# Optimization experiments

Hardware: AMD Instinct MI355X
Metric: run time of the kernel (lower is better)

Reference implementation:

```python
import itertools
import jax, jax.numpy as jnp
import numpy as np

DIM = 3; N_NEIGH = 4096; N_CH = 64
BASIS_RANK_MAX = 2; SELF_TP_RANK_MAX = 2; H_MAX_RANK = 2  # layer=1 -> h_max_rank=2
R_CUT = 5.0  # Bessel radial-basis cutoff (assumed)

def find_combinations(a_max, b_max, s):
    if s > a_max + b_max or s < 0:
        return []
    return [(a, s - a) for a in range(max(0, s - b_max), min(a_max, s) + 1)]

def contraction_is_valid(n_in, n_out):
    # can only reduce legs pairwise (metric contraction)
    return n_in >= n_out and (n_in - n_out) % 2 == 0

def _pairings(legs):
    if not legs:
        yield []
        return
    a = legs[0]
    for i in range(1, len(legs)):
        for rest in _pairings(legs[1:i] + legs[i + 1:]):
            yield [(a, legs[i])] + rest

def contraction_einsums(a, b, c_out):
    # all distinct pairwise contractions of an (a+b)-leg Cartesian tensor down to c_out free legs
    n = a + b
    letters = 'defghijklm'
    eqs = []
    for contracted in itertools.combinations(range(n), n - c_out):
        free = [l for l in range(n) if l not in contracted]
        for match in _pairings(list(contracted)):
            lab = {}
            cnt = 0
            for l in free:
                lab[l] = letters[cnt]; cnt += 1
            for (p, q) in match:
                lab[p] = lab[q] = letters[cnt]; cnt += 1
            s1 = 'nc' + ''.join(lab[l] for l in range(a))
            s2 = 'nc' + ''.join(lab[l] for l in range(a, n))
            so = 'nc' + ''.join(lab[l] for l in free)
            eqs.append(f'{s1},{s2}->{so}')
    return eqs

def tensor_prod(r, order):
    # repeated outer product of unit vectors: (N, dim^order); order 0 -> ones (N,)
    if order == 0:
        return jnp.ones((r.shape[0],), r.dtype)
    out = r
    for _ in range(order - 1):
        out = jnp.einsum('n...,nd->n...d', out, r)
    return out

def e_rbf(r, n):
    # Bessel/sinc radial basis: sqrt(2/c) sin(n pi r / c) / r
    return jnp.sqrt(2.0 / R_CUT) * jnp.sin(n * jnp.pi * r / R_CUT) / r

def setup_inputs() -> dict:
    key = jax.random.key(0)
    ks = jax.random.split(key, 5)
    return {
        'h0': jax.random.normal(ks[0], (N_NEIGH, N_CH), jnp.float32),
        'h1': jax.random.normal(ks[1], (N_NEIGH, N_CH, DIM), jnp.float32),
        'h2': jax.random.normal(ks[2], (N_NEIGH, N_CH, DIM, DIM), jnp.float32),
        'rel_poss': jax.random.normal(ks[3], (N_NEIGH, DIM), jnp.float32),
        'channel_weights': jax.random.normal(ks[4], (BASIS_RANK_MAX + 1, N_NEIGH, N_CH, N_CH), jnp.float32),
    }

def _forward(h0, h1, h2, rel_poss, channel_weights):
    h = [h0, h1, h2]
    dists = jnp.linalg.norm(rel_poss, axis=-1)                  # (N,)
    nrp = rel_poss / dists.reshape(-1, 1)                       # unit vectors (N, 3)
    # channel mixing computed but unused downstream in the original forward (dead code, kept faithful)
    _ = [jnp.einsum('ijk,ik...->ij...', channel_weights[r], h[r]) for r in range(BASIS_RANK_MAX + 1)]
    r_base = [tensor_prod(nrp, k) for k in range(SELF_TP_RANK_MAX + 1)]
    n_vals = jnp.arange(1, N_CH + 1, dtype=jnp.float32)[:, None]  # (C, 1)
    radial = e_rbf(dists, n_vals).reshape(N_NEIGH, N_CH)          # faithful reshape (as in source, not a transpose)
    r_tensors = [jnp.einsum('ij,i...->ij...', radial, r_base[k]) for k in range(SELF_TP_RANK_MAX + 1)]
    tensors_out = [[] for _ in range(BASIS_RANK_MAX + 1)]
    for n_indices in range(0, H_MAX_RANK + SELF_TP_RANK_MAX + 1):
        for (a, b) in find_combinations(H_MAX_RANK, SELF_TP_RANK_MAX, n_indices):
            for br in range(BASIS_RANK_MAX + 1):
                if contraction_is_valid(n_indices, br):
                    for eq in contraction_einsums(a, b, br):
                        tensors_out[br].append(jnp.einsum(eq, h[a], r_tensors[b]))
    a_set = []
    for lst in tensors_out:
        stacked = jnp.stack(lst)                    # (paths, N, C, 3^rank)
        a_set.append(jnp.einsum('ijk...->k...', stacked))  # sum paths + neighbours -> (C, 3^rank)
    return tuple(a_set)

def reference(h0, h1, h2, rel_poss, channel_weights):
    return _forward(h0, h1, h2, rel_poss, channel_weights)
```

## Files before the change

kernel.cpp:

```cpp
#include <hip/hip_runtime.h>
#include <math.h>

#define NN 4096
#define NC 64
#define OUT_ELEMS 832

__global__ void zero_kernel(float* __restrict__ out) {
    int i = blockIdx.x * blockDim.x + threadIdx.x;
    if (i < OUT_ELEMS) out[i] = 0.0f;
}

__launch_bounds__(256)
__global__ void basis_kernel(const float* __restrict__ h0,
                             const float* __restrict__ h1,
                             const float* __restrict__ h2,
                             const float* __restrict__ rel,
                             float* __restrict__ out) {
    const int t = threadIdx.x;
    const int c = t & 63;
    const int mlane = t >> 6;
    const int m0 = blockIdx.x * 16;

    float a0 = 0.0f;
    float a1[3] = {0.f, 0.f, 0.f};
    float a2[9] = {0.f,0.f,0.f,0.f,0.f,0.f,0.f,0.f,0.f};

    for (int mi = mlane; mi < 16; mi += 4) {
        const int m = m0 + mi;

        const int mo = ((m & 63) << 6) | c;
        const float nval = (float)((m >> 6) + 1);

        float rx = rel[3*mo+0], ry = rel[3*mo+1], rz = rel[3*mo+2];
        float dmo = sqrtf(rx*rx + ry*ry + rz*rz);
        float arg = nval * 3.14159265358979323846f * dmo * 0.2f;
        float R = 0.6324555320336759f * sinf(arg) / dmo;

        float px = rel[3*m+0], py = rel[3*m+1], pz = rel[3*m+2];
        float dm = sqrtf(px*px + py*py + pz*pz);
        float inv = 1.0f / dm;
        float ux = px*inv, uy = py*inv, uz = pz*inv;
        float uu = ux*ux + uy*uy + uz*uz;
        float opu = 1.0f + uu;

        const int base = m * NC + c;
        float s0 = h0[base];
        const float* vp = h1 + 3*base;
        float v0 = vp[0], v1 = vp[1], v2 = vp[2];
        const float* Hp = h2 + 9*base;
        float H00=Hp[0], H01=Hp[1], H02=Hp[2];
        float H10=Hp[3], H11=Hp[4], H12=Hp[5];
        float H20=Hp[6], H21=Hp[7], H22=Hp[8];

        float dot1 = v0*ux + v1*uy + v2*uz;
        float tr2  = H00 + H11 + H22;
        float w0 = H00*ux + H01*uy + H02*uz;
        float w1 = H10*ux + H11*uy + H12*uz;
        float w2 = H20*ux + H21*uy + H22*uz;
        float t0 = H00*ux + H10*uy + H20*uz;
        float t1 = H01*ux + H11*uy + H21*uz;
        float t2 = H02*ux + H12*uy + H22*uz;
        float quad = w0*ux + w1*uy + w2*uz;

        a0 += R * (s0*opu + dot1 + tr2*opu + 2.0f*quad);

        float k1 = s0 + 2.0f*dot1 + tr2;
        a1[0] += R * (k1*ux + opu*v0 + t0 + w0);
        a1[1] += R * (k1*uy + opu*v1 + t1 + w1);
        a1[2] += R * (k1*uz + opu*v2 + t2 + w2);

        float k2 = s0 + tr2;
        float q0 = v0 + 2.0f*(t0 + w0);
        float q1 = v1 + 2.0f*(t1 + w1);
        float q2 = v2 + 2.0f*(t2 + w2);
        float u[3]  = {ux, uy, uz};
        float q[3]  = {q0, q1, q2};
        float Hm[9] = {H00,H01,H02,H10,H11,H12,H20,H21,H22};
        #pragma unroll
        for (int d = 0; d < 3; ++d)
            #pragma unroll
            for (int e = 0; e < 3; ++e)
                a2[3*d+e] += R * (k2*u[d]*u[e] + q[d]*u[e] + opu*Hm[3*d+e]);
    }

    __shared__ float red[256][14];
    red[t][0] = a0;
    red[t][1] = a1[0]; red[t][2] = a1[1]; red[t][3] = a1[2];
    #pragma unroll
    for (int k = 0; k < 9; ++k) red[t][4+k] = a2[k];
    __syncthreads();

    if (t < 64) {
        #pragma unroll
        for (int k = 0; k < 13; ++k) {
            float s = red[t][k] + red[t+64][k] + red[t+128][k] + red[t+192][k];
            int idx = (k == 0) ? t
                    : (k < 4)  ? (64 + t*3 + (k-1))
                               : (256 + t*9 + (k-4));
            atomicAdd(&out[idx], s);
        }
    }
}

extern "C" void kernel_launch(void* const* d_in, const int* in_sizes, int n_in,
                              void* d_out, int out_size, void* d_ws, size_t ws_size,
                              hipStream_t stream) {
    const float* h0  = (const float*)d_in[0];
    const float* h1  = (const float*)d_in[1];
    const float* h2  = (const float*)d_in[2];
    const float* rel = (const float*)d_in[3];
    float* out = (float*)d_out;

    zero_kernel<<<4, 256, 0, stream>>>(out);
    basis_kernel<<<NN / 16, 256, 0, stream>>>(h0, h1, h2, rel, out);
}
```

Baseline: 302.6 us.

## Replace atomic reduction with two-stage workspace reduction and more blocks

Each block now writes its per-channel partial sums to a workspace instead of issuing atomicAdds into the 832-element output. A second kernel sums the 512 partials per element and writes the output directly, so the zero-init kernel is no longer needed. The grid is doubled to 512 blocks of 8 neighbours each to raise occupancy. This removes atomic contention on the same addresses, at the cost of an extra launch and a serial 512-step loop per thread in stage 2 that runs on only 832 threads.

```diff
diff --git a/kernel.cpp b/kernel.cpp
--- a/kernel.cpp
+++ b/kernel.cpp
@@ -3,29 +3,26 @@
 
 #define NN 4096
 #define NC 64
+#define NPART 13
 #define OUT_ELEMS 832
-
-__global__ void zero_kernel(float* __restrict__ out) {
-    int i = blockIdx.x * blockDim.x + threadIdx.x;
-    if (i < OUT_ELEMS) out[i] = 0.0f;
-}
+#define NBLK 512
 
 __launch_bounds__(256)
-__global__ void basis_kernel(const float* __restrict__ h0,
+__global__ void basis_stage1(const float* __restrict__ h0,
                              const float* __restrict__ h1,
                              const float* __restrict__ h2,
                              const float* __restrict__ rel,
-                             float* __restrict__ out) {
+                             float* __restrict__ ws) {
     const int t = threadIdx.x;
     const int c = t & 63;
     const int mlane = t >> 6;
-    const int m0 = blockIdx.x * 16;
+    const int m0 = blockIdx.x * 8;
 
     float a0 = 0.0f;
     float a1[3] = {0.f, 0.f, 0.f};
     float a2[9] = {0.f,0.f,0.f,0.f,0.f,0.f,0.f,0.f,0.f};
 
-    for (int mi = mlane; mi < 16; mi += 4) {
+    for (int mi = mlane; mi < 8; mi += 4) {
         const int m = m0 + mi;
 
         const int mo = ((m & 63) << 6) | c;
@@ -90,16 +87,29 @@
     for (int k = 0; k < 9; ++k) red[t][4+k] = a2[k];
     __syncthreads();
 
-    if (t < 64) {
-        #pragma unroll
-        for (int k = 0; k < 13; ++k) {
-            float s = red[t][k] + red[t+64][k] + red[t+128][k] + red[t+192][k];
-            int idx = (k == 0) ? t
-                    : (k < 4)  ? (64 + t*3 + (k-1))
-                               : (256 + t*9 + (k-4));
-            atomicAdd(&out[idx], s);
-        }
+    float* wsb = ws + blockIdx.x * (NPART * NC);
+    for (int i = t; i < NPART * NC; i += 256) {
+        int k = i >> 6;
+        int cc = i & 63;
+        wsb[i] = red[cc][k] + red[cc+64][k] + red[cc+128][k] + red[cc+192][k];
     }
+}
+
+__launch_bounds__(256)
+__global__ void basis_stage2(const float* __restrict__ ws,
+                             float* __restrict__ out) {
+    int i = blockIdx.x * blockDim.x + threadIdx.x;
+    if (i >= NPART * NC) return;
+    float s = 0.0f;
+    #pragma unroll 8
+    for (int b = 0; b < NBLK; ++b)
+        s += ws[b * (NPART * NC) + i];
+    int k = i >> 6;
+    int c = i & 63;
+    int idx = (k == 0) ? c
+            : (k < 4)  ? (64 + c*3 + (k-1))
+                       : (256 + c*9 + (k-4));
+    out[idx] = s;
 }
 
 extern "C" void kernel_launch(void* const* d_in, const int* in_sizes, int n_in,
@@ -110,7 +120,8 @@
     const float* h2  = (const float*)d_in[2];
     const float* rel = (const float*)d_in[3];
     float* out = (float*)d_out;
+    float* ws  = (float*)d_ws;
 
-    zero_kernel<<<4, 256, 0, stream>>>(out);
-    basis_kernel<<<NN / 16, 256, 0, stream>>>(h0, h1, h2, rel, out);
+    basis_stage1<<<NBLK, 256, 0, stream>>>(h0, h1, h2, rel, ws);
+    basis_stage2<<<(NPART * NC + 255) / 256, 256, 0, stream>>>(ws, out);
 }
```

Result: faster. 267.8 us (-11.5%).
